# Performance work log

Measured on AMD Instinct MI355X. Metric: run time of the kernel, lower is better.

## Reference

```python
import jax, jax.numpy as jnp
import numpy as np

N, E, P = 50000, 1600000, 500000
IN_DIM, HID, OUT = 512, 128, 64
EPS = 1e-5


def setup_inputs() -> dict:
    key = jax.random.key(0)
    ks = jax.random.split(key, 16)
    d = {}
    d['x'] = jax.random.normal(ks[0], (N, IN_DIM), dtype=jnp.float32)
    d['ei'] = jax.random.randint(ks[1], (2, E), 0, N, dtype=jnp.int32)
    d['src'] = jax.random.randint(ks[2], (P,), 0, N, dtype=jnp.int32)
    d['dst'] = jax.random.randint(ks[3], (P,), 0, N, dtype=jnp.int32)
    # GCNConv layer 1 params
    d['W1'] = jax.random.normal(ks[4], (IN_DIM, HID), dtype=jnp.float32) / np.sqrt(IN_DIM)
    d['b1'] = jnp.zeros((HID,), jnp.float32)
    d['bn1_gamma'] = jnp.ones((HID,), jnp.float32)
    d['bn1_beta'] = jnp.zeros((HID,), jnp.float32)
    d['bn1_mean'] = jnp.zeros((HID,), jnp.float32)
    d['bn1_var'] = jnp.ones((HID,), jnp.float32)
    # GCNConv layer 2 params
    d['W2'] = jax.random.normal(ks[5], (HID, OUT), dtype=jnp.float32) / np.sqrt(HID)
    d['b2'] = jnp.zeros((OUT,), jnp.float32)
    d['bn2_gamma'] = jnp.ones((OUT,), jnp.float32)
    d['bn2_beta'] = jnp.zeros((OUT,), jnp.float32)
    d['bn2_mean'] = jnp.zeros((OUT,), jnp.float32)
    d['bn2_var'] = jnp.ones((OUT,), jnp.float32)
    # edge head MLP
    d['hW1'] = jax.random.normal(ks[6], (2 * OUT, OUT), dtype=jnp.float32) / np.sqrt(2 * OUT)
    d['hb1'] = jnp.zeros((OUT,), jnp.float32)
    d['hW2'] = jax.random.normal(ks[7], (OUT, 1), dtype=jnp.float32) / np.sqrt(OUT)
    d['hb2'] = jnp.zeros((1,), jnp.float32)
    return d


def gcn_conv(x, ei, W, b):
    """PyG-style GCNConv: add self-loops, symmetric deg^-1/2 normalization."""
    xw = x @ W  # [N, F]
    row, col = ei[0], ei[1]
    ones = jnp.ones((ei.shape[1],), x.dtype)
    deg = jax.ops.segment_sum(ones, col, num_segments=N) + 1.0  # +1 for self-loop
    dinv = jax.lax.rsqrt(deg)
    norm = dinv[row] * dinv[col]  # [E]
    agg = jax.ops.segment_sum(norm[:, None] * xw[row], col, num_segments=N)
    # self-loop contribution: dinv[i]^2 * xw[i]
    return agg + (dinv * dinv)[:, None] * xw + b


def bn_eval(x, gamma, beta, mean, var):
    return (x - mean) * jax.lax.rsqrt(var + EPS) * gamma + beta


def reference(x, ei, src, dst, W1, b1, bn1_gamma, bn1_beta, bn1_mean, bn1_var,
              W2, b2, bn2_gamma, bn2_beta, bn2_mean, bn2_var, hW1, hb1, hW2, hb2):
    h = jax.nn.relu(bn_eval(gcn_conv(x, ei, W1, b1), bn1_gamma, bn1_beta, bn1_mean, bn1_var))
    # dropout is identity in eval mode
    z = jax.nn.relu(bn_eval(gcn_conv(h, ei, W2, b2), bn2_gamma, bn2_beta, bn2_mean, bn2_var))
    pair = jnp.concatenate([z[src], z[dst]], axis=1)  # [P, 2*OUT]
    hmid = jax.nn.relu(pair @ hW1 + hb1)
    logits = hmid @ hW2 + hb2  # [P, 1]
    return jax.nn.sigmoid(logits).squeeze(-1)
```

## Files before the change

kernel.cpp:

```cpp
#include <hip/hip_runtime.h>
#include <math.h>


typedef __attribute__((ext_vector_type(8))) short short8x;
typedef __attribute__((ext_vector_type(8))) _Float16 half8x;
typedef __attribute__((ext_vector_type(4))) float f32x4;
typedef __attribute__((ext_vector_type(2))) unsigned int uint2x;
typedef __attribute__((ext_vector_type(2))) float float2x;

__device__ __forceinline__ unsigned short f2bf(float f) {
  unsigned int u = __float_as_uint(f);
  unsigned int r = u + 0x7FFFu + ((u >> 16) & 1u);
  return (unsigned short)(r >> 16);
}
__device__ __forceinline__ unsigned short f2h(float f) {
  union { _Float16 h; unsigned short u; } cv;
  cv.h = (_Float16)f;
  return cv.u;
}


__global__ void zero_int_kernel(int* __restrict__ p, int n) {
  int i = blockIdx.x * blockDim.x + threadIdx.x;
  if (i < n) p[i] = 0;
}

__global__ __launch_bounds__(256) void binA_hist_kernel(const int* __restrict__ col,
                                                        int* __restrict__ bucket_count, int E,
                                                        int NBK) {
  __shared__ int hist[256];
  const int tid = threadIdx.x;
  hist[tid] = 0;
  __syncthreads();
  const int base = blockIdx.x * 4096;
#pragma unroll
  for (int j = 0; j < 16; ++j) {
    int i = base + j * 256 + tid;
    if (i < E) atomicAdd(&hist[((unsigned int)col[i]) >> 8], 1);
  }
  __syncthreads();
  if (tid < NBK) {
    int h = hist[tid];
    if (h) atomicAdd(&bucket_count[tid], h);
  }
}

__global__ __launch_bounds__(256) void scan_buckets_kernel(const int* __restrict__ bucket_count,
                                                           int* __restrict__ bucket_start,
                                                           int* __restrict__ bcur,
                                                           int* __restrict__ offs_n, int NBK,
                                                           int E) {
  __shared__ int ws[4];
  const int tid = threadIdx.x;
  const int lane = tid & 63;
  const int wid = tid >> 6;
  int v = (tid < NBK) ? bucket_count[tid] : 0;
  int incl = v;
#pragma unroll
  for (int d = 1; d < 64; d <<= 1) {
    int t = __shfl_up(incl, d, 64);
    if (lane >= d) incl += t;
  }
  if (lane == 63) ws[wid] = incl;
  __syncthreads();
  int woff = 0;
#pragma unroll
  for (int w = 0; w < 4; ++w)
    if (w < wid) woff += ws[w];
  int excl = woff + incl - v;
  if (tid < NBK) {
    bucket_start[tid] = excl;
    bcur[tid] = excl;
  }
  if (tid == 0) {
    bucket_start[NBK] = E;
    *offs_n = E;
  }
}

__global__ __launch_bounds__(256) void binA_scatter_kernel(const int* __restrict__ row,
                                                           const int* __restrict__ col,
                                                           int* __restrict__ bcur,
                                                           unsigned int* __restrict__ staging,
                                                           int E, int NBK) {
  __shared__ int hist[256];
  const int tid = threadIdx.x;
  hist[tid] = 0;
  __syncthreads();
  const int base = blockIdx.x * 4096;
  unsigned int payload[16];
  int bk[16];
#pragma unroll
  for (int j = 0; j < 16; ++j) {
    int i = base + j * 256 + tid;
    if (i < E) {
      unsigned int c = (unsigned int)__builtin_nontemporal_load(&col[i]);
      unsigned int r = (unsigned int)__builtin_nontemporal_load(&row[i]);
      payload[j] = (c << 16) | r;
      bk[j] = (int)(c >> 8);
      atomicAdd(&hist[bk[j]], 1);
    } else {
      bk[j] = -1;
    }
  }
  __syncthreads();
  if (tid < NBK) {
    int h = hist[tid];
    hist[tid] = h ? atomicAdd(&bcur[tid], h) : 0;
  }
  __syncthreads();
#pragma unroll
  for (int j = 0; j < 16; ++j) {
    if (bk[j] >= 0) {
      int p = atomicAdd(&hist[bk[j]], 1);
      staging[p] = payload[j];
    }
  }
}

__global__ __launch_bounds__(256) void binB1_kernel(const unsigned int* __restrict__ staging,
                                                    const int* __restrict__ bucket_start,
                                                    int* __restrict__ offs,
                                                    float* __restrict__ dinv, int N) {
  __shared__ int cnt[256];
  __shared__ int ws[4];
  const int b = blockIdx.x;
  const int n0 = b * 256;
  const int tid = threadIdx.x;
  cnt[tid] = 0;
  __syncthreads();
  const int s = bucket_start[b];
  const int e = bucket_start[b + 1];
  for (int t = s + tid; t < e; t += 256) {
    atomicAdd(&cnt[(staging[t] >> 16) & 255u], 1);
  }
  __syncthreads();
  const int deg = cnt[tid];
  const int lane = tid & 63;
  const int wid = tid >> 6;
  int incl = deg;
#pragma unroll
  for (int d = 1; d < 64; d <<= 1) {
    int t = __shfl_up(incl, d, 64);
    if (lane >= d) incl += t;
  }
  if (lane == 63) ws[wid] = incl;
  __syncthreads();
  int woff = 0;
#pragma unroll
  for (int w = 0; w < 4; ++w)
    if (w < wid) woff += ws[w];
  const int excl = woff + incl - deg;
  const int node = n0 + tid;
  if (node < N) {
    offs[node] = s + excl;
    dinv[node] = rsqrtf((float)deg + 1.0f);
  }
}

__global__ __launch_bounds__(512) void binB2_kernel(const unsigned int* __restrict__ staging,
                                                    const int* __restrict__ offs,
                                                    const int* __restrict__ bucket_start,
                                                    const float* __restrict__ dinv,
                                                    unsigned int* __restrict__ csr, int N) {
  __shared__ int cur[256];
  const int b = blockIdx.x;
  const int n0 = b * 256;
  const int tid = threadIdx.x;
  if (tid < 256 && n0 + tid < N) cur[tid] = offs[n0 + tid];
  __syncthreads();
  const int s = bucket_start[b];
  const int e = bucket_start[b + 1];
  for (int t = s + tid; t < e; t += 512) {
    unsigned int v = __builtin_nontemporal_load(&staging[t]);
    int cl = (int)((v >> 16) & 255u);
    unsigned int r = v & 0xFFFFu;
    unsigned int wd = f2bf(dinv[r]);
    int p = atomicAdd(&cur[cl], 1);
    csr[p] = (wd << 16) | r;
  }
}

__global__ __launch_bounds__(256) void prep_all_kernel(const float* __restrict__ W1,
                                                       const float* __restrict__ W2,
                                                       const float* __restrict__ hW1,
                                                       unsigned short* __restrict__ bfW1,
                                                       unsigned short* __restrict__ bfW2,
                                                       unsigned short* __restrict__ bfH) {
  int idx = blockIdx.x * blockDim.x + threadIdx.x;
  const float* W;
  unsigned short* out;
  int K, N, base, mode;
  if (idx < 8192) {
    W = W1; out = bfW1; K = 512; N = 128; base = 0; mode = 0;
  } else if (idx < 9216) {
    W = W2; out = bfW2; K = 128; N = 64; base = 8192; mode = 0;
  } else if (idx < 10240) {
    W = hW1; out = bfH; K = 64; N = 128; base = 9216; mode = 1;
  } else {
    return;
  }
  int id = idx - base;
  int lane = id & 63;
  int t = id >> 6;
  int KS = K / 32;
  int ks = t % KS;
  int nt = t / KS;
  int n = nt * 16 + (lane & 15);
  int k0 = ks * 32 + (lane >> 4) * 8;
  unsigned short* o = out + (size_t)id * 8;
#pragma unroll
  for (int j = 0; j < 8; ++j) {
    int k = k0 + j;
    float v;
    if (mode == 0)
      v = W[(size_t)k * N + n];
    else
      v = (n < 64) ? W[(size_t)k * 64 + n] : W[(size_t)(64 + k) * 64 + (n - 64)];
    o[j] = f2bf(v);
  }
}

template <int K, int N, bool ABF16, bool OUTF16>
__global__ __launch_bounds__(256) void mfma_gemm_kernel(const void* __restrict__ Ap,
                                                        const unsigned short* __restrict__ Bfrag,
                                                        unsigned short* __restrict__ Cout, int M) {
  constexpr int KS = K / 32;
  constexpr int NT = N / 16;
  const int lane = threadIdx.x & 63;
  const int wid = threadIdx.x >> 6;
  const int quad = lane >> 4;
  const int lc = lane & 15;
  const int mbase = blockIdx.x * 128 + wid * 32;
  if (mbase >= M) return;

  f32x4 acc[2][NT];
#pragma unroll
  for (int mt = 0; mt < 2; ++mt)
#pragma unroll
    for (int nt = 0; nt < NT; ++nt) acc[mt][nt] = (f32x4){0.f, 0.f, 0.f, 0.f};

  int r0 = mbase + lc;
  int r1 = mbase + 16 + lc;
  if (r0 >= M) r0 = M - 1;
  if (r1 >= M) r1 = M - 1;

#pragma unroll
  for (int ks = 0; ks < KS; ++ks) {
    const int k0 = ks * 32 + quad * 8;
    short8x a[2];
    if constexpr (ABF16) {
      const unsigned short* A = (const unsigned short*)Ap;
      a[0] = *(const short8x*)(A + (size_t)r0 * K + k0);
      a[1] = *(const short8x*)(A + (size_t)r1 * K + k0);
    } else {
      const float* A = (const float*)Ap;
      const float4* p0 = (const float4*)(A + (size_t)r0 * K + k0);
      const float4* p1 = (const float4*)(A + (size_t)r1 * K + k0);
      float4 u0 = p0[0], v0 = p0[1];
      float4 u1 = p1[0], v1 = p1[1];
      short8x t0, t1;
      t0[0] = (short)f2bf(u0.x); t0[1] = (short)f2bf(u0.y);
      t0[2] = (short)f2bf(u0.z); t0[3] = (short)f2bf(u0.w);
      t0[4] = (short)f2bf(v0.x); t0[5] = (short)f2bf(v0.y);
      t0[6] = (short)f2bf(v0.z); t0[7] = (short)f2bf(v0.w);
      t1[0] = (short)f2bf(u1.x); t1[1] = (short)f2bf(u1.y);
      t1[2] = (short)f2bf(u1.z); t1[3] = (short)f2bf(u1.w);
      t1[4] = (short)f2bf(v1.x); t1[5] = (short)f2bf(v1.y);
      t1[6] = (short)f2bf(v1.z); t1[7] = (short)f2bf(v1.w);
      a[0] = t0;
      a[1] = t1;
    }
#pragma unroll
    for (int nt = 0; nt < NT; ++nt) {
      short8x b = *(const short8x*)(Bfrag + (((size_t)nt * KS + ks) * 64 + lane) * 8);
      acc[0][nt] = __builtin_amdgcn_mfma_f32_16x16x32_bf16(a[0], b, acc[0][nt], 0, 0, 0);
      acc[1][nt] = __builtin_amdgcn_mfma_f32_16x16x32_bf16(a[1], b, acc[1][nt], 0, 0, 0);
    }
  }

#pragma unroll
  for (int mt = 0; mt < 2; ++mt)
#pragma unroll
    for (int nt = 0; nt < NT; ++nt)
#pragma unroll
      for (int reg = 0; reg < 4; ++reg) {
        int row = mbase + mt * 16 + quad * 4 + reg;
        if (row < M) {
          float v = acc[mt][nt][reg];
          Cout[(size_t)row * N + nt * 16 + lc] = OUTF16 ? f2h(v) : f2bf(v);
        }
      }
}

template <int RD>
__global__ __launch_bounds__(256) void agg_fast_kernel(
    const unsigned short* __restrict__ xw, const int* __restrict__ offs,
    const unsigned int* __restrict__ csr, const float* __restrict__ dinv,
    const float* __restrict__ bias, const float* __restrict__ gamma,
    const float* __restrict__ beta, const float* __restrict__ mean,
    const float* __restrict__ var, unsigned short* __restrict__ out, int N) {
  constexpr int G = RD / 2;
  constexpr int NPB = 256 / G;
  const int li = threadIdx.x % G;
  const int i = blockIdx.x * NPB + threadIdx.x / G;
  if (i >= N) return;
  const uint2x* xw64 = (const uint2x*)xw;
  const float di = dinv[i];
  const int s = offs[i], e = offs[i + 1];
  float2x acc0 = {0.f, 0.f};
  float2x acc1 = {0.f, 0.f};
  int t = s;
  for (; t + 16 <= e; t += 16) {
    unsigned int ent[16];
#pragma unroll
    for (int j = 0; j < 16; ++j) ent[j] = __builtin_nontemporal_load(&csr[t + j]);
    uint2x gv[16];
#pragma unroll
    for (int j = 0; j < 16; ++j) gv[j] = xw64[(size_t)(ent[j] & 0xFFFFu) * G + li];
#pragma unroll
    for (int j = 0; j < 16; ++j) {
      float w = __uint_as_float(ent[j] & 0xFFFF0000u);
      float2x wv = {w, w};
      float2x x0 = {__uint_as_float(gv[j].x << 16), __uint_as_float(gv[j].x & 0xFFFF0000u)};
      float2x x1 = {__uint_as_float(gv[j].y << 16), __uint_as_float(gv[j].y & 0xFFFF0000u)};
      acc0 = __builtin_elementwise_fma(wv, x0, acc0);
      acc1 = __builtin_elementwise_fma(wv, x1, acc1);
    }
  }
  for (; t + 4 <= e; t += 4) {
    unsigned int ent[4];
#pragma unroll
    for (int j = 0; j < 4; ++j) ent[j] = __builtin_nontemporal_load(&csr[t + j]);
    uint2x gv[4];
#pragma unroll
    for (int j = 0; j < 4; ++j) gv[j] = xw64[(size_t)(ent[j] & 0xFFFFu) * G + li];
#pragma unroll
    for (int j = 0; j < 4; ++j) {
      float w = __uint_as_float(ent[j] & 0xFFFF0000u);
      float2x wv = {w, w};
      float2x x0 = {__uint_as_float(gv[j].x << 16), __uint_as_float(gv[j].x & 0xFFFF0000u)};
      float2x x1 = {__uint_as_float(gv[j].y << 16), __uint_as_float(gv[j].y & 0xFFFF0000u)};
      acc0 = __builtin_elementwise_fma(wv, x0, acc0);
      acc1 = __builtin_elementwise_fma(wv, x1, acc1);
    }
  }
  for (; t < e; ++t) {
    unsigned int ee = __builtin_nontemporal_load(&csr[t]);
    uint2x gv = xw64[(size_t)(ee & 0xFFFFu) * G + li];
    float w = __uint_as_float(ee & 0xFFFF0000u);
    float2x wv = {w, w};
    float2x x0 = {__uint_as_float(gv.x << 16), __uint_as_float(gv.x & 0xFFFF0000u)};
    float2x x1 = {__uint_as_float(gv.y << 16), __uint_as_float(gv.y & 0xFFFF0000u)};
    acc0 = __builtin_elementwise_fma(wv, x0, acc0);
    acc1 = __builtin_elementwise_fma(wv, x1, acc1);
  }
  const int f0 = 4 * li;
  uint2x sv = xw64[(size_t)i * G + li];
  float sl0 = __uint_as_float(sv.x << 16), sh0 = __uint_as_float(sv.x & 0xFFFF0000u);
  float sl1 = __uint_as_float(sv.y << 16), sh1 = __uint_as_float(sv.y & 0xFFFF0000u);
  const float dd = di * di;
  float v0 = di * acc0.x + dd * sl0 + bias[f0 + 0];
  float v1 = di * acc0.y + dd * sh0 + bias[f0 + 1];
  float v2 = di * acc1.x + dd * sl1 + bias[f0 + 2];
  float v3 = di * acc1.y + dd * sh1 + bias[f0 + 3];
  v0 = (v0 - mean[f0 + 0]) * rsqrtf(var[f0 + 0] + 1e-5f) * gamma[f0 + 0] + beta[f0 + 0];
  v1 = (v1 - mean[f0 + 1]) * rsqrtf(var[f0 + 1] + 1e-5f) * gamma[f0 + 1] + beta[f0 + 1];
  v2 = (v2 - mean[f0 + 2]) * rsqrtf(var[f0 + 2] + 1e-5f) * gamma[f0 + 2] + beta[f0 + 2];
  v3 = (v3 - mean[f0 + 3]) * rsqrtf(var[f0 + 3] + 1e-5f) * gamma[f0 + 3] + beta[f0 + 3];
  uint2x packed;
  packed.x = (unsigned int)f2bf(fmaxf(v0, 0.f)) | ((unsigned int)f2bf(fmaxf(v1, 0.f)) << 16);
  packed.y = (unsigned int)f2bf(fmaxf(v2, 0.f)) | ((unsigned int)f2bf(fmaxf(v3, 0.f)) << 16);
  ((uint2x*)out)[(size_t)i * G + li] = packed;
}

__global__ __launch_bounds__(256) void head2_kernel(
    const unsigned short* __restrict__ zh, const int* __restrict__ src,
    const int* __restrict__ dst, const float* __restrict__ hb1,
    const float* __restrict__ hw2, const float* __restrict__ hb2,
    float* __restrict__ out, int P) {
  const int lane = threadIdx.x & 63;
  const int lc = lane & 15;
  const int quad = lane >> 4;
  float b1v[16], w2v[16];
#pragma unroll
  for (int t = 0; t < 16; ++t) {
    b1v[t] = hb1[quad * 16 + t];
    w2v[t] = hw2[quad * 16 + t];
  }
  const float bias2 = hb2[0];
  const int nchunks = (P + 15) / 16;
  const int gw = blockIdx.x * 4 + (threadIdx.x >> 6);
  const int nw = gridDim.x * 4;

  for (int ch = gw; ch < nchunks; ch += nw) {
    int p = ch * 16 + lc;
    int pc = p < P ? p : P - 1;
    int s = __builtin_nontemporal_load(&src[pc]);
    int d = __builtin_nontemporal_load(&dst[pc]);
    const half8x* pa = (const half8x*)(zh + (size_t)s * 128 + quad * 16);
    const half8x* pb = (const half8x*)(zh + (size_t)d * 128 + 64 + quad * 16);
    half8x a0 = pa[0], a1 = pa[1];
    half8x b0 = pb[0], b1 = pb[1];
    float acc = 0.f;
#pragma unroll
    for (int t = 0; t < 8; ++t) {
      float hm = fmaxf((float)a0[t] + (float)b0[t] + b1v[t], 0.f);
      acc = fmaf(hm, w2v[t], acc);
    }
#pragma unroll
    for (int t = 0; t < 8; ++t) {
      float hm = fmaxf((float)a1[t] + (float)b1[t] + b1v[8 + t], 0.f);
      acc = fmaf(hm, w2v[8 + t], acc);
    }
    acc += __shfl_xor(acc, 16, 64);
    acc += __shfl_xor(acc, 32, 64);
    if (quad == 0 && p < P) {
      float o = 1.0f / (1.0f + __expf(-(acc + bias2)));
      __builtin_nontemporal_store(o, &out[p]);
    }
  }
}


extern "C" void kernel_launch(void* const* d_in, const int* in_sizes, int n_in,
                              void* d_out, int out_size, void* d_ws, size_t ws_size,
                              hipStream_t stream) {
  const float* x = (const float*)d_in[0];
  const int* ei = (const int*)d_in[1];
  const int* src = (const int*)d_in[2];
  const int* dst = (const int*)d_in[3];
  const float* W1 = (const float*)d_in[4];
  const float* b1 = (const float*)d_in[5];
  const float* g1 = (const float*)d_in[6];
  const float* be1 = (const float*)d_in[7];
  const float* mu1 = (const float*)d_in[8];
  const float* va1 = (const float*)d_in[9];
  const float* W2 = (const float*)d_in[10];
  const float* b2 = (const float*)d_in[11];
  const float* g2 = (const float*)d_in[12];
  const float* be2 = (const float*)d_in[13];
  const float* mu2 = (const float*)d_in[14];
  const float* va2 = (const float*)d_in[15];
  const float* hW1 = (const float*)d_in[16];
  const float* hb1 = (const float*)d_in[17];
  const float* hW2 = (const float*)d_in[18];
  const float* hb2 = (const float*)d_in[19];
  float* out = (float*)d_out;

  const int N = in_sizes[0] / 512;
  const int E = in_sizes[1] / 2;
  const int P = in_sizes[2];
  const int* row = ei;
  const int* col = ei + E;
  const int NBK = (N + 255) / 256;
  const int NAB = (E + 4095) / 4096;

  char* wp = (char*)d_ws;
  auto alloc = [&](size_t bytes) {
    char* p = wp;
    wp += (bytes + 255) & ~(size_t)255;
    return p;
  };
  unsigned short* xw1 = (unsigned short*)alloc((size_t)N * 128 * 2);
  unsigned short* h = (unsigned short*)alloc((size_t)N * 128 * 2);
  unsigned short* xw2 = (unsigned short*)alloc((size_t)N * 64 * 2);
  unsigned short* z = (unsigned short*)alloc((size_t)N * 64 * 2);
  unsigned short* zh = (unsigned short*)alloc((size_t)N * 128 * 2);
  float* dinv = (float*)alloc((size_t)N * 4);
  int* offs = (int*)alloc((size_t)(N + 1) * 4);
  unsigned int* csr = (unsigned int*)alloc((size_t)E * 4);
  unsigned int* staging = (unsigned int*)alloc((size_t)E * 4);
  int* bucket_count = (int*)alloc((size_t)NBK * 4);
  int* bucket_start = (int*)alloc((size_t)(NBK + 1) * 4);
  int* bcur = (int*)alloc((size_t)NBK * 4);
  unsigned short* bfW1 = (unsigned short*)alloc(512 * 128 * 2);
  unsigned short* bfW2 = (unsigned short*)alloc(128 * 64 * 2);
  unsigned short* bfH = (unsigned short*)alloc(128 * 64 * 2);
  (void)ws_size;
  (void)n_in;
  (void)out_size;

  hipLaunchKernelGGL(zero_int_kernel, dim3((NBK + 255) / 256), dim3(256), 0, stream, bucket_count,
                     NBK);
  hipLaunchKernelGGL(binA_hist_kernel, dim3(NAB), dim3(256), 0, stream, col, bucket_count, E, NBK);
  hipLaunchKernelGGL(scan_buckets_kernel, dim3(1), dim3(256), 0, stream, bucket_count,
                     bucket_start, bcur, offs + N, NBK, E);
  hipLaunchKernelGGL(binA_scatter_kernel, dim3(NAB), dim3(256), 0, stream, row, col, bcur, staging,
                     E, NBK);
  hipLaunchKernelGGL(binB1_kernel, dim3(NBK), dim3(256), 0, stream, staging, bucket_start, offs,
                     dinv, N);
  hipLaunchKernelGGL(binB2_kernel, dim3(NBK), dim3(512), 0, stream, staging, offs, bucket_start,
                     dinv, csr, N);

  hipLaunchKernelGGL(prep_all_kernel, dim3(40), dim3(256), 0, stream, W1, W2, hW1, bfW1, bfW2,
                     bfH);

  hipLaunchKernelGGL((mfma_gemm_kernel<512, 128, false, false>), dim3((N + 127) / 128), dim3(256),
                     0, stream, x, bfW1, xw1, N);
  hipLaunchKernelGGL((agg_fast_kernel<64>), dim3((N + 7) / 8), dim3(256), 0, stream, xw1, offs,
                     csr, dinv, b1, g1, be1, mu1, va1, h, N);

  hipLaunchKernelGGL((mfma_gemm_kernel<128, 64, true, false>), dim3((N + 127) / 128), dim3(256), 0,
                     stream, h, bfW2, xw2, N);
  hipLaunchKernelGGL((agg_fast_kernel<32>), dim3((N + 15) / 16), dim3(256), 0, stream, xw2, offs,
                     csr, dinv, b2, g2, be2, mu2, va2, z, N);

  hipLaunchKernelGGL((mfma_gemm_kernel<64, 128, true, true>), dim3((N + 127) / 128), dim3(256), 0,
                     stream, z, bfH, zh, N);
  hipLaunchKernelGGL(head2_kernel, dim3(2048), dim3(256), 0, stream, zh, src, dst, hb1, hW2, hb2,
                     out, P);
}
```

Measured before the change: 400.3 us.

## Co-schedule weight prep with histogram and layer-1 GEMM with edge scatter

Measured after the change: 395.4 us. About the same (-1.2%).

```diff
diff --git a/kernel.cpp b/kernel.cpp
--- a/kernel.cpp
+++ b/kernel.cpp
@@ -25,10 +25,55 @@
   if (i < n) p[i] = 0;
 }
 
-__global__ __launch_bounds__(256) void binA_hist_kernel(const int* __restrict__ col,
-                                                        int* __restrict__ bucket_count, int E,
-                                                        int NBK) {
+__device__ __forceinline__ void prep_body(int idx, const float* __restrict__ W1,
+                                          const float* __restrict__ W2,
+                                          const float* __restrict__ hW1,
+                                          unsigned short* __restrict__ bfW1,
+                                          unsigned short* __restrict__ bfW2,
+                                          unsigned short* __restrict__ bfH) {
+  const float* W;
+  unsigned short* out;
+  int K, N, base, mode;
+  if (idx < 8192) {
+    W = W1; out = bfW1; K = 512; N = 128; base = 0; mode = 0;
+  } else if (idx < 9216) {
+    W = W2; out = bfW2; K = 128; N = 64; base = 8192; mode = 0;
+  } else if (idx < 10240) {
+    W = hW1; out = bfH; K = 64; N = 128; base = 9216; mode = 1;
+  } else {
+    return;
+  }
+  int id = idx - base;
+  int lane = id & 63;
+  int t = id >> 6;
+  int KS = K / 32;
+  int ks = t % KS;
+  int nt = t / KS;
+  int n = nt * 16 + (lane & 15);
+  int k0 = ks * 32 + (lane >> 4) * 8;
+  unsigned short* o = out + (size_t)id * 8;
+#pragma unroll
+  for (int j = 0; j < 8; ++j) {
+    int k = k0 + j;
+    float v;
+    if (mode == 0)
+      v = W[(size_t)k * N + n];
+    else
+      v = (n < 64) ? W[(size_t)k * 64 + n] : W[(size_t)(64 + k) * 64 + (n - 64)];
+    o[j] = f2bf(v);
+  }
+}
+
+__global__ __launch_bounds__(256) void hist_prep_kernel(
+    const int* __restrict__ col, int* __restrict__ bucket_count, int E, int NBK, int NAB,
+    const float* __restrict__ W1, const float* __restrict__ W2, const float* __restrict__ hW1,
+    unsigned short* __restrict__ bfW1, unsigned short* __restrict__ bfW2,
+    unsigned short* __restrict__ bfH) {
   __shared__ int hist[256];
+  if ((int)blockIdx.x >= NAB) {
+    prep_body(((int)blockIdx.x - NAB) * 256 + threadIdx.x, W1, W2, hW1, bfW1, bfW2, bfH);
+    return;
+  }
   const int tid = threadIdx.x;
   hist[tid] = 0;
   __syncthreads();
@@ -78,160 +123,18 @@
   }
 }
 
-__global__ __launch_bounds__(256) void binA_scatter_kernel(const int* __restrict__ row,
-                                                           const int* __restrict__ col,
-                                                           int* __restrict__ bcur,
-                                                           unsigned int* __restrict__ staging,
-                                                           int E, int NBK) {
-  __shared__ int hist[256];
-  const int tid = threadIdx.x;
-  hist[tid] = 0;
-  __syncthreads();
-  const int base = blockIdx.x * 4096;
-  unsigned int payload[16];
-  int bk[16];
-#pragma unroll
-  for (int j = 0; j < 16; ++j) {
-    int i = base + j * 256 + tid;
-    if (i < E) {
-      unsigned int c = (unsigned int)__builtin_nontemporal_load(&col[i]);
-      unsigned int r = (unsigned int)__builtin_nontemporal_load(&row[i]);
-      payload[j] = (c << 16) | r;
-      bk[j] = (int)(c >> 8);
-      atomicAdd(&hist[bk[j]], 1);
-    } else {
-      bk[j] = -1;
-    }
-  }
-  __syncthreads();
-  if (tid < NBK) {
-    int h = hist[tid];
-    hist[tid] = h ? atomicAdd(&bcur[tid], h) : 0;
-  }
-  __syncthreads();
-#pragma unroll
-  for (int j = 0; j < 16; ++j) {
-    if (bk[j] >= 0) {
-      int p = atomicAdd(&hist[bk[j]], 1);
-      staging[p] = payload[j];
-    }
-  }
-}
-
-__global__ __launch_bounds__(256) void binB1_kernel(const unsigned int* __restrict__ staging,
-                                                    const int* __restrict__ bucket_start,
-                                                    int* __restrict__ offs,
-                                                    float* __restrict__ dinv, int N) {
-  __shared__ int cnt[256];
-  __shared__ int ws[4];
-  const int b = blockIdx.x;
-  const int n0 = b * 256;
-  const int tid = threadIdx.x;
-  cnt[tid] = 0;
-  __syncthreads();
-  const int s = bucket_start[b];
-  const int e = bucket_start[b + 1];
-  for (int t = s + tid; t < e; t += 256) {
-    atomicAdd(&cnt[(staging[t] >> 16) & 255u], 1);
-  }
-  __syncthreads();
-  const int deg = cnt[tid];
+template <int K, int N, bool ABF16, bool OUTF16>
+__device__ __forceinline__ void gemm_body(const void* __restrict__ Ap,
+                                          const unsigned short* __restrict__ Bfrag,
+                                          unsigned short* __restrict__ Cout, int M, int bid,
+                                          int tid) {
+  constexpr int KS = K / 32;
+  constexpr int NT = N / 16;
   const int lane = tid & 63;
   const int wid = tid >> 6;
-  int incl = deg;
-#pragma unroll
-  for (int d = 1; d < 64; d <<= 1) {
-    int t = __shfl_up(incl, d, 64);
-    if (lane >= d) incl += t;
-  }
-  if (lane == 63) ws[wid] = incl;
-  __syncthreads();
-  int woff = 0;
-#pragma unroll
-  for (int w = 0; w < 4; ++w)
-    if (w < wid) woff += ws[w];
-  const int excl = woff + incl - deg;
-  const int node = n0 + tid;
-  if (node < N) {
-    offs[node] = s + excl;
-    dinv[node] = rsqrtf((float)deg + 1.0f);
-  }
-}
-
-__global__ __launch_bounds__(512) void binB2_kernel(const unsigned int* __restrict__ staging,
-                                                    const int* __restrict__ offs,
-                                                    const int* __restrict__ bucket_start,
-                                                    const float* __restrict__ dinv,
-                                                    unsigned int* __restrict__ csr, int N) {
-  __shared__ int cur[256];
-  const int b = blockIdx.x;
-  const int n0 = b * 256;
-  const int tid = threadIdx.x;
-  if (tid < 256 && n0 + tid < N) cur[tid] = offs[n0 + tid];
-  __syncthreads();
-  const int s = bucket_start[b];
-  const int e = bucket_start[b + 1];
-  for (int t = s + tid; t < e; t += 512) {
-    unsigned int v = __builtin_nontemporal_load(&staging[t]);
-    int cl = (int)((v >> 16) & 255u);
-    unsigned int r = v & 0xFFFFu;
-    unsigned int wd = f2bf(dinv[r]);
-    int p = atomicAdd(&cur[cl], 1);
-    csr[p] = (wd << 16) | r;
-  }
-}
-
-__global__ __launch_bounds__(256) void prep_all_kernel(const float* __restrict__ W1,
-                                                       const float* __restrict__ W2,
-                                                       const float* __restrict__ hW1,
-                                                       unsigned short* __restrict__ bfW1,
-                                                       unsigned short* __restrict__ bfW2,
-                                                       unsigned short* __restrict__ bfH) {
-  int idx = blockIdx.x * blockDim.x + threadIdx.x;
-  const float* W;
-  unsigned short* out;
-  int K, N, base, mode;
-  if (idx < 8192) {
-    W = W1; out = bfW1; K = 512; N = 128; base = 0; mode = 0;
-  } else if (idx < 9216) {
-    W = W2; out = bfW2; K = 128; N = 64; base = 8192; mode = 0;
-  } else if (idx < 10240) {
-    W = hW1; out = bfH; K = 64; N = 128; base = 9216; mode = 1;
-  } else {
-    return;
-  }
-  int id = idx - base;
-  int lane = id & 63;
-  int t = id >> 6;
-  int KS = K / 32;
-  int ks = t % KS;
-  int nt = t / KS;
-  int n = nt * 16 + (lane & 15);
-  int k0 = ks * 32 + (lane >> 4) * 8;
-  unsigned short* o = out + (size_t)id * 8;
-#pragma unroll
-  for (int j = 0; j < 8; ++j) {
-    int k = k0 + j;
-    float v;
-    if (mode == 0)
-      v = W[(size_t)k * N + n];
-    else
-      v = (n < 64) ? W[(size_t)k * 64 + n] : W[(size_t)(64 + k) * 64 + (n - 64)];
-    o[j] = f2bf(v);
-  }
-}
-
-template <int K, int N, bool ABF16, bool OUTF16>
-__global__ __launch_bounds__(256) void mfma_gemm_kernel(const void* __restrict__ Ap,
-                                                        const unsigned short* __restrict__ Bfrag,
-                                                        unsigned short* __restrict__ Cout, int M) {
-  constexpr int KS = K / 32;
-  constexpr int NT = N / 16;
-  const int lane = threadIdx.x & 63;
-  const int wid = threadIdx.x >> 6;
   const int quad = lane >> 4;
   const int lc = lane & 15;
-  const int mbase = blockIdx.x * 128 + wid * 32;
+  const int mbase = bid * 128 + wid * 32;
   if (mbase >= M) return;
 
   f32x4 acc[2][NT];
@@ -293,6 +196,119 @@
       }
 }
 
+template <int K, int N, bool ABF16, bool OUTF16>
+__global__ __launch_bounds__(256) void mfma_gemm_kernel(const void* __restrict__ Ap,
+                                                        const unsigned short* __restrict__ Bfrag,
+                                                        unsigned short* __restrict__ Cout, int M) {
+  gemm_body<K, N, ABF16, OUTF16>(Ap, Bfrag, Cout, M, blockIdx.x, threadIdx.x);
+}
+
+__global__ __launch_bounds__(256) void scatter_gemm_kernel(
+    const int* __restrict__ row, const int* __restrict__ col, int* __restrict__ bcur,
+    unsigned int* __restrict__ staging, int E, int NBK, int NAB, const float* __restrict__ x,
+    const unsigned short* __restrict__ bfW1, unsigned short* __restrict__ xw1, int M) {
+  __shared__ int hist[256];
+  if ((int)blockIdx.x >= NAB) {
+    gemm_body<512, 128, false, false>(x, bfW1, xw1, M, (int)blockIdx.x - NAB, threadIdx.x);
+    return;
+  }
+  const int tid = threadIdx.x;
+  hist[tid] = 0;
+  __syncthreads();
+  const int base = blockIdx.x * 4096;
+  unsigned int payload[16];
+  int bk[16];
+#pragma unroll
+  for (int j = 0; j < 16; ++j) {
+    int i = base + j * 256 + tid;
+    if (i < E) {
+      unsigned int c = (unsigned int)__builtin_nontemporal_load(&col[i]);
+      unsigned int r = (unsigned int)__builtin_nontemporal_load(&row[i]);
+      payload[j] = (c << 16) | r;
+      bk[j] = (int)(c >> 8);
+      atomicAdd(&hist[bk[j]], 1);
+    } else {
+      bk[j] = -1;
+    }
+  }
+  __syncthreads();
+  if (tid < NBK) {
+    int h = hist[tid];
+    hist[tid] = h ? atomicAdd(&bcur[tid], h) : 0;
+  }
+  __syncthreads();
+#pragma unroll
+  for (int j = 0; j < 16; ++j) {
+    if (bk[j] >= 0) {
+      int p = atomicAdd(&hist[bk[j]], 1);
+      staging[p] = payload[j];
+    }
+  }
+}
+
+__global__ __launch_bounds__(256) void binB1_kernel(const unsigned int* __restrict__ staging,
+                                                    const int* __restrict__ bucket_start,
+                                                    int* __restrict__ offs,
+                                                    float* __restrict__ dinv, int N) {
+  __shared__ int cnt[256];
+  __shared__ int ws[4];
+  const int b = blockIdx.x;
+  const int n0 = b * 256;
+  const int tid = threadIdx.x;
+  cnt[tid] = 0;
+  __syncthreads();
+  const int s = bucket_start[b];
+  const int e = bucket_start[b + 1];
+  for (int t = s + tid; t < e; t += 256) {
+    atomicAdd(&cnt[(staging[t] >> 16) & 255u], 1);
+  }
+  __syncthreads();
+  const int deg = cnt[tid];
+  const int lane = tid & 63;
+  const int wid = tid >> 6;
+  int incl = deg;
+#pragma unroll
+  for (int d = 1; d < 64; d <<= 1) {
+    int t = __shfl_up(incl, d, 64);
+    if (lane >= d) incl += t;
+  }
+  if (lane == 63) ws[wid] = incl;
+  __syncthreads();
+  int woff = 0;
+#pragma unroll
+  for (int w = 0; w < 4; ++w)
+    if (w < wid) woff += ws[w];
+  const int excl = woff + incl - deg;
+  const int node = n0 + tid;
+  if (node < N) {
+    offs[node] = s + excl;
+    dinv[node] = rsqrtf((float)deg + 1.0f);
+  }
+}
+
+__global__ __launch_bounds__(512) void binB2_kernel(const unsigned int* __restrict__ staging,
+                                                    const int* __restrict__ offs,
+                                                    const int* __restrict__ bucket_start,
+                                                    const float* __restrict__ dinv,
+                                                    unsigned int* __restrict__ csr, int N) {
+  __shared__ int cur[256];
+  const int b = blockIdx.x;
+  const int n0 = b * 256;
+  const int tid = threadIdx.x;
+  if (tid < 256 && n0 + tid < N) cur[tid] = offs[n0 + tid];
+  __syncthreads();
+  const int s = bucket_start[b];
+  const int e = bucket_start[b + 1];
+  for (int t = s + tid; t < e; t += 512) {
+    unsigned int v = __builtin_nontemporal_load(&staging[t]);
+    int cl = (int)((v >> 16) & 255u);
+    unsigned int r = v & 0xFFFFu;
+    unsigned int wd = f2bf(dinv[r]);
+    int p = atomicAdd(&cur[cl], 1);
+    csr[p] = (wd << 16) | r;
+  }
+}
+
 template <int RD>
 __global__ __launch_bounds__(256) void agg_fast_kernel(
     const unsigned short* __restrict__ xw, const int* __restrict__ offs,
@@ -390,34 +406,54 @@
   }
   const float bias2 = hb2[0];
   const int nchunks = (P + 15) / 16;
+  const int npair = (nchunks + 1) / 2;
   const int gw = blockIdx.x * 4 + (threadIdx.x >> 6);
   const int nw = gridDim.x * 4;
 
-  for (int ch = gw; ch < nchunks; ch += nw) {
-    int p = ch * 16 + lc;
-    int pc = p < P ? p : P - 1;
-    int s = __builtin_nontemporal_load(&src[pc]);
-    int d = __builtin_nontemporal_load(&dst[pc]);
-    const half8x* pa = (const half8x*)(zh + (size_t)s * 128 + quad * 16);
-    const half8x* pb = (const half8x*)(zh + (size_t)d * 128 + 64 + quad * 16);
-    half8x a0 = pa[0], a1 = pa[1];
-    half8x b0 = pb[0], b1 = pb[1];
-    float acc = 0.f;
+  for (int cp = gw; cp < npair; cp += nw) {
+    const int ch0 = cp * 2;
+    const int ch1 = ch0 + 1;
+    const bool has1 = ch1 < nchunks;
+    int p0 = ch0 * 16 + lc;
+    int p1 = (has1 ? ch1 : ch0) * 16 + lc;
+    int pc0 = p0 < P ? p0 : P - 1;
+    int pc1 = p1 < P ? p1 : P - 1;
+    int s0 = __builtin_nontemporal_load(&src[pc0]);
+    int d0 = __builtin_nontemporal_load(&dst[pc0]);
+    int s1 = __builtin_nontemporal_load(&src[pc1]);
+    int d1 = __builtin_nontemporal_load(&dst[pc1]);
+    const half8x* pa0 = (const half8x*)(zh + (size_t)s0 * 128 + quad * 16);
+    const half8x* pb0 = (const half8x*)(zh + (size_t)d0 * 128 + 64 + quad * 16);
+    const half8x* pa1 = (const half8x*)(zh + (size_t)s1 * 128 + quad * 16);
+    const half8x* pb1 = (const half8x*)(zh + (size_t)d1 * 128 + 64 + quad * 16);
+    half8x a00 = pa0[0], a01 = pa0[1];
+    half8x b00 = pb0[0], b01 = pb0[1];
+    half8x a10 = pa1[0], a11 = pa1[1];
+    half8x b10 = pb1[0], b11 = pb1[1];
+    float acc0 = 0.f, acc1 = 0.f;
 #pragma unroll
     for (int t = 0; t < 8; ++t) {
-      float hm = fmaxf((float)a0[t] + (float)b0[t] + b1v[t], 0.f);
-      acc = fmaf(hm, w2v[t], acc);
+      acc0 = fmaf(fmaxf((float)a00[t] + (float)b00[t] + b1v[t], 0.f), w2v[t], acc0);
+      acc1 = fmaf(fmaxf((float)a10[t] + (float)b10[t] + b1v[t], 0.f), w2v[t], acc1);
     }
 #pragma unroll
     for (int t = 0; t < 8; ++t) {
-      float hm = fmaxf((float)a1[t] + (float)b1[t] + b1v[8 + t], 0.f);
-      acc = fmaf(hm, w2v[8 + t], acc);
-    }
-    acc += __shfl_xor(acc, 16, 64);
-    acc += __shfl_xor(acc, 32, 64);
-    if (quad == 0 && p < P) {
-      float o = 1.0f / (1.0f + __expf(-(acc + bias2)));
-      __builtin_nontemporal_store(o, &out[p]);
+      acc0 = fmaf(fmaxf((float)a01[t] + (float)b01[t] + b1v[8 + t], 0.f), w2v[8 + t], acc0);
+      acc1 = fmaf(fmaxf((float)a11[t] + (float)b11[t] + b1v[8 + t], 0.f), w2v[8 + t], acc1);
+    }
+    acc0 += __shfl_xor(acc0, 16, 64);
+    acc0 += __shfl_xor(acc0, 32, 64);
+    acc1 += __shfl_xor(acc1, 16, 64);
+    acc1 += __shfl_xor(acc1, 32, 64);
+    if (quad == 0) {
+      if (p0 < P) {
+        float o = 1.0f / (1.0f + __expf(-(acc0 + bias2)));
+        __builtin_nontemporal_store(o, &out[p0]);
+      }
+      if (has1 && p1 < P) {
+        float o = 1.0f / (1.0f + __expf(-(acc1 + bias2)));
+        __builtin_nontemporal_store(o, &out[p1]);
+      }
     }
   }
 }
@@ -455,6 +491,7 @@
   const int* col = ei + E;
   const int NBK = (N + 255) / 256;
   const int NAB = (E + 4095) / 4096;
+  const int NGB = (N + 127) / 128;
 
   char* wp = (char*)d_ws;
   auto alloc = [&](size_t bytes) {
@@ -483,31 +520,27 @@
 
   hipLaunchKernelGGL(zero_int_kernel, dim3((NBK + 255) / 256), dim3(256), 0, stream, bucket_count,
                      NBK);
-  hipLaunchKernelGGL(binA_hist_kernel, dim3(NAB), dim3(256), 0, stream, col, bucket_count, E, NBK);
+  hipLaunchKernelGGL(hist_prep_kernel, dim3(NAB + 40), dim3(256), 0, stream, col, bucket_count, E,
+                     NBK, NAB, W1, W2, hW1, bfW1, bfW2, bfH);
   hipLaunchKernelGGL(scan_buckets_kernel, dim3(1), dim3(256), 0, stream, bucket_count,
                      bucket_start, bcur, offs + N, NBK, E);
-  hipLaunchKernelGGL(binA_scatter_kernel, dim3(NAB), dim3(256), 0, stream, row, col, bcur, staging,
-                     E, NBK);
+  hipLaunchKernelGGL(scatter_gemm_kernel, dim3(NAB + NGB), dim3(256), 0, stream, row, col, bcur,
+                     staging, E, NBK, NAB, x, bfW1, xw1, N);
   hipLaunchKernelGGL(binB1_kernel, dim3(NBK), dim3(256), 0, stream, staging, bucket_start, offs,
                      dinv, N);
   hipLaunchKernelGGL(binB2_kernel, dim3(NBK), dim3(512), 0, stream, staging, offs, bucket_start,
                      dinv, csr, N);
 
-  hipLaunchKernelGGL(prep_all_kernel, dim3(40), dim3(256), 0, stream, W1, W2, hW1, bfW1, bfW2,
-                     bfH);
-
-  hipLaunchKernelGGL((mfma_gemm_kernel<512, 128, false, false>), dim3((N + 127) / 128), dim3(256),
-                     0, stream, x, bfW1, xw1, N);
   hipLaunchKernelGGL((agg_fast_kernel<64>), dim3((N + 7) / 8), dim3(256), 0, stream, xw1, offs,
                      csr, dinv, b1, g1, be1, mu1, va1, h, N);
 
-  hipLaunchKernelGGL((mfma_gemm_kernel<128, 64, true, false>), dim3((N + 127) / 128), dim3(256), 0,
-                     stream, h, bfW2, xw2, N);
+  hipLaunchKernelGGL((mfma_gemm_kernel<128, 64, true, false>), dim3(NGB), dim3(256), 0, stream, h,
+                     bfW2, xw2, N);
   hipLaunchKernelGGL((agg_fast_kernel<32>), dim3((N + 15) / 16), dim3(256), 0, stream, xw2, offs,
                      csr, dinv, b2, g2, be2, mu2, va2, z, N);
 
-  hipLaunchKernelGGL((mfma_gemm_kernel<64, 128, true, true>), dim3((N + 127) / 128), dim3(256), 0,
-                     stream, z, bfH, zh, N);
-  hipLaunchKernelGGL(head2_kernel, dim3(2048), dim3(256), 0, stream, zh, src, dst, hb1, hW2, hb2,
+  hipLaunchKernelGGL((mfma_gemm_kernel<64, 128, true, true>), dim3(NGB), dim3(256), 0, stream, z,
+                     bfH, zh, N);
+  hipLaunchKernelGGL(head2_kernel, dim3(4096), dim3(256), 0, stream, zh, src, dst, hb1, hW2, hb2,
                      out, P);
 }
```
